# Kernel tuning notes

Measured on AMD Instinct MI355X. Metric: run time of the kernel, lower is better.

Reference implementation:

```python
import jax, jax.numpy as jnp
import numpy as np

SIZE = 1024      # codebook size
DIM = 64         # latent_dim
TOPK = 3
BETA_C = 0.25
LEGACY = False

def setup_inputs() -> dict:
    key = jax.random.key(0)
    kz, ke = jax.random.split(key)
    z = jax.random.normal(kz, (16, 64, 64, DIM), dtype=jnp.float32)
    # nn.Embedding init: uniform(-1/size, 1/size)
    emb = jax.random.uniform(ke, (SIZE, DIM), minval=-1.0 / SIZE, maxval=1.0 / SIZE, dtype=jnp.float32)
    return {"z": z, "emb": emb}

def reference(z, emb):
    zf = z.reshape(-1, DIM)                                  # [N, D]
    # squared euclidean distances via matmul expansion: [N, SIZE]
    d = (jnp.sum(zf ** 2, axis=1, keepdims=True)
         + jnp.sum(emb ** 2, axis=1)
         - 2.0 * (zf @ emb.T))
    neg_d, topk_idx = jax.lax.top_k(-d, TOPK)                # smallest distances -> [N, K]
    # direct gather instead of one-hot matmul (same math)
    z_q = jnp.mean(emb[topk_idx], axis=1).reshape(z.shape)   # [N,K,D] -> [N,D] -> z.shape
    if LEGACY:
        loss = (jnp.mean((jax.lax.stop_gradient(z_q) - z) ** 2)
                + BETA_C * jnp.mean((z_q - jax.lax.stop_gradient(z)) ** 2))
    else:
        loss = (BETA_C * jnp.mean((jax.lax.stop_gradient(z_q) - z) ** 2)
                + jnp.mean((z_q - jax.lax.stop_gradient(z)) ** 2))
    # one-hot encodings are part of the module's return signature
    topk_encodings = jax.nn.one_hot(topk_idx, SIZE, dtype=z.dtype)   # [N, K, SIZE]
    e_mean = jnp.mean(topk_encodings, axis=(0, 1))                   # [SIZE]
    perplexity = jnp.exp(-jnp.sum(e_mean * jnp.log(e_mean + 1e-10)))
    z_q_st = z + jax.lax.stop_gradient(z_q - z)              # straight-through estimator
    return (z_q_st, loss, perplexity, topk_encodings, topk_idx)
```

## Files before the change

### kernel.cpp

```cpp
#include <hip/hip_runtime.h>
#include <math.h>

#define N_ROWS 65536
#define CB 1024
#define SPLITS 4
#define JS (CB / SPLITS)

typedef float v4f __attribute__((ext_vector_type(4)));

__device__ __forceinline__ float tree_sum64_sq(const float* x) {
#pragma clang fp contract(off)
    float sq[64];
#pragma unroll
    for (int i = 0; i < 64; ++i) sq[i] = x[i] * x[i];
    float s[16];
#pragma unroll
    for (int l = 0; l < 16; ++l) s[l] = (sq[l] + sq[l + 16]) + (sq[l + 32] + sq[l + 48]);
    float t[8];
#pragma unroll
    for (int l = 0; l < 8; ++l) t[l] = s[l] + s[l + 8];
    float u[4];
#pragma unroll
    for (int l = 0; l < 4; ++l) u[l] = t[l] + t[l + 4];
    float v0 = u[0] + u[2];
    float v1 = u[1] + u[3];
    return v0 + v1;
}

__device__ __forceinline__ void top3_insert(float d, int j,
                                            float& v0, float& v1, float& v2,
                                            int& i0, int& i1, int& i2) {
    bool b0 = d < v0, b1 = d < v1, b2 = d < v2;
    v2 = b1 ? v1 : (b2 ? d : v2);
    i2 = b1 ? i1 : (b2 ? j : i2);
    v1 = b0 ? v0 : (b1 ? d : v1);
    i1 = b0 ? i0 : (b1 ? j : i1);
    v0 = b0 ? d : v0;
    i0 = b0 ? j : i0;
}

__global__ __launch_bounds__(256) void prep_kernel(const float* __restrict__ emb,
                                                   float* __restrict__ B,
                                                   int* __restrict__ hist,
                                                   float* __restrict__ lossAcc) {
    int j = blockIdx.x * 256 + threadIdx.x;
    if (j >= CB) return;
    float e[64];
    const float4* e4 = (const float4*)(emb + (size_t)j * 64);
#pragma unroll
    for (int k = 0; k < 16; ++k) {
        float4 v = e4[k];
        e[4 * k] = v.x; e[4 * k + 1] = v.y; e[4 * k + 2] = v.z; e[4 * k + 3] = v.w;
    }
    B[j] = tree_sum64_sq(e);
    hist[j] = 0;
    if (j == 0) *lossAcc = 0.0f;
}

__global__ __launch_bounds__(256) void score_kernel(const float* __restrict__ z,
                                                    const float* __restrict__ emb,
                                                    const float* __restrict__ B,
                                                    float* __restrict__ out0,
                                                    float* __restrict__ out3f,
                                                    float* __restrict__ out4,
                                                    int* __restrict__ hist,
                                                    float* __restrict__ lossAcc) {
    __shared__ float sD[SPLITS][64][3];
    __shared__ int   sI[SPLITS][64][3];

    int t = threadIdx.x;
    int r = t & 63;
    int split = __builtin_amdgcn_readfirstlane(t >> 6);
    int row = blockIdx.x * 64 + r;

    float zr[64];
    const float4* z4 = (const float4*)(z + (size_t)row * 64);
#pragma unroll
    for (int k = 0; k < 16; ++k) {
        float4 v = z4[k];
        zr[4 * k] = v.x; zr[4 * k + 1] = v.y; zr[4 * k + 2] = v.z; zr[4 * k + 3] = v.w;
    }
    float A = tree_sum64_sq(zr);

    float v0 = 3.402823466e38f, v1 = 3.402823466e38f, v2 = 3.402823466e38f;
    int i0 = 0, i1 = 0, i2 = 0;
    int jbase = split * JS;

#pragma unroll 2
    for (int jj = 0; jj < JS; ++jj) {
        int j = jbase + jj;
        const float4* e4 = (const float4*)(emb + (size_t)j * 64);
        float Bj = B[j];
        float acc = 0.0f;
#pragma unroll
        for (int k = 0; k < 16; ++k) {
            float4 e = e4[k];
            acc = fmaf(zr[4 * k],     e.x, acc);
            acc = fmaf(zr[4 * k + 1], e.y, acc);
            acc = fmaf(zr[4 * k + 2], e.z, acc);
            acc = fmaf(zr[4 * k + 3], e.w, acc);
        }
        float d = (A + Bj) - 2.0f * acc;
        top3_insert(d, j, v0, v1, v2, i0, i1, i2);
    }

    sD[split][r][0] = v0; sD[split][r][1] = v1; sD[split][r][2] = v2;
    sI[split][r][0] = i0; sI[split][r][1] = i1; sI[split][r][2] = i2;
    __syncthreads();

    if (t < 64) {
        float m0 = 3.402823466e38f, m1 = 3.402823466e38f, m2 = 3.402823466e38f;
        int j0 = 0, j1 = 0, j2 = 0;
#pragma unroll
        for (int s = 0; s < SPLITS; ++s) {
#pragma unroll
            for (int u = 0; u < 3; ++u)
                top3_insert(sD[s][r][u], sI[s][r][u], m0, m1, m2, j0, j1, j2);
        }

        size_t sb = (size_t)row * 3 * 1024;
        out3f[sb + j0]        = 1.0f;
        out3f[sb + 1024 + j1] = 1.0f;
        out3f[sb + 2048 + j2] = 1.0f;

        const float4* e0q = (const float4*)(emb + (size_t)j0 * 64);
        const float4* e1q = (const float4*)(emb + (size_t)j1 * 64);
        const float4* e2q = (const float4*)(emb + (size_t)j2 * 64);
        v4f* o4 = (v4f*)(out0 + (size_t)row * 64);

        float lsum = 0.0f;
#pragma unroll
        for (int k4 = 0; k4 < 16; ++k4) {
            float4 a = e0q[k4], b = e1q[k4], c = e2q[k4];
            float zx = zr[4 * k4], zy = zr[4 * k4 + 1];
            float zz = zr[4 * k4 + 2], zw = zr[4 * k4 + 3];
            v4f st;
            float zq, df;
            zq = ((a.x + b.x) + c.x) / 3.0f; df = zq - zx; st.x = zx + df; lsum = fmaf(df, df, lsum);
            zq = ((a.y + b.y) + c.y) / 3.0f; df = zq - zy; st.y = zy + df; lsum = fmaf(df, df, lsum);
            zq = ((a.z + b.z) + c.z) / 3.0f; df = zq - zz; st.z = zz + df; lsum = fmaf(df, df, lsum);
            zq = ((a.w + b.w) + c.w) / 3.0f; df = zq - zw; st.w = zw + df; lsum = fmaf(df, df, lsum);
            o4[k4] = st;
        }

        size_t ob = (size_t)row * 3;
        out4[ob]     = (float)j0;
        out4[ob + 1] = (float)j1;
        out4[ob + 2] = (float)j2;
        atomicAdd(&hist[j0], 1);
        atomicAdd(&hist[j1], 1);
        atomicAdd(&hist[j2], 1);

#pragma unroll
        for (int off = 32; off >= 1; off >>= 1) lsum += __shfl_down(lsum, off);
        if ((t & 63) == 0) atomicAdd(lossAcc, lsum);
    }
}

__global__ __launch_bounds__(256) void finalize_kernel(const int* __restrict__ hist,
                                                       const float* __restrict__ lossAcc,
                                                       float* __restrict__ out1,
                                                       float* __restrict__ out2) {
    __shared__ float red[256];
    int t = threadIdx.x;
    float local = 0.0f;
    for (int b = t; b < CB; b += 256) {
        float em = (float)hist[b] / 196608.0f;
        local += em * logf(em + 1e-10f);
    }
    red[t] = local;
    __syncthreads();
    for (int s = 128; s >= 1; s >>= 1) {
        if (t < s) red[t] += red[t + s];
        __syncthreads();
    }
    if (t == 0) {
        *out2 = expf(-red[0]);
        float m = *lossAcc / 4194304.0f;
        *out1 = 0.25f * m + m;
    }
}

extern "C" void kernel_launch(void* const* d_in, const int* in_sizes, int n_in,
                              void* d_out, int out_size, void* d_ws, size_t ws_size,
                              hipStream_t stream) {
    const float* z   = (const float*)d_in[0];
    const float* emb = (const float*)d_in[1];

    float* out  = (float*)d_out;
    float* out0 = out;
    float* out1 = out + 4194304;
    float* out2 = out + 4194305;
    float* out3 = out + 4194306;
    float* out4 = out + 4194306 + 201326592ll;

    int*   hist    = (int*)d_ws;
    float* lossAcc = (float*)((char*)d_ws + 4096);
    float* B       = (float*)((char*)d_ws + 8192);

    prep_kernel<<<4, 256, 0, stream>>>(emb, B, hist, lossAcc);
    hipMemsetAsync(out3, 0, (size_t)N_ROWS * 3 * CB * sizeof(float), stream);
    score_kernel<<<N_ROWS / 64, 256, 0, stream>>>(z, emb, B, out0, out3, out4,
                                                  hist, lossAcc);
    finalize_kernel<<<1, 256, 0, stream>>>(hist, lossAcc, out1, out2);
}
```

Before: 1.092 ms.

## Overlap one-hot zero-fill with scoring via filler blocks and per-slice flags

Drops the separate hipMemsetAsync of the large one-hot output and folds the zeroing into the main kernel. Extra filler blocks zero 4 row-group slices each, so the compute-bound scoring overlaps the bandwidth-bound fill. Per-slice flags and acquire/release atomics order the zeroing before the one-hot writes. If a filler has not claimed a slice in time, the scoring block takes it over and writes the full one-hot rows itself. This adds spin-wait synchronization, a launch_bounds occupancy hint, and the risk of stalls or deadlock if fillers are scheduled late.

New measurement: 1.201 ms. 1.1x slower.

```diff
diff --git a/kernel.cpp b/kernel.cpp
--- a/kernel.cpp
+++ b/kernel.cpp
@@ -5,6 +5,8 @@
 #define CB 1024
 #define SPLITS 4
 #define JS (CB / SPLITS)
+#define NFILLER 256
+#define SLICE_F 196608
 
 typedef float v4f __attribute__((ext_vector_type(4)));
 
@@ -42,7 +44,8 @@
 __global__ __launch_bounds__(256) void prep_kernel(const float* __restrict__ emb,
                                                    float* __restrict__ B,
                                                    int* __restrict__ hist,
-                                                   float* __restrict__ lossAcc) {
+                                                   float* __restrict__ lossAcc,
+                                                   int* __restrict__ flags) {
     int j = blockIdx.x * 256 + threadIdx.x;
     if (j >= CB) return;
     float e[64];
@@ -54,24 +57,60 @@
     }
     B[j] = tree_sum64_sq(e);
     hist[j] = 0;
+    flags[j] = 0;
     if (j == 0) *lossAcc = 0.0f;
 }
 
-__global__ __launch_bounds__(256) void score_kernel(const float* __restrict__ z,
-                                                    const float* __restrict__ emb,
-                                                    const float* __restrict__ B,
-                                                    float* __restrict__ out0,
-                                                    float* __restrict__ out3f,
-                                                    float* __restrict__ out4,
-                                                    int* __restrict__ hist,
-                                                    float* __restrict__ lossAcc) {
+__global__ __launch_bounds__(256, 5) void main_kernel(const float* __restrict__ z,
+                                                      const float* __restrict__ emb,
+                                                      const float* __restrict__ B,
+                                                      float* __restrict__ out0,
+                                                      float* __restrict__ out3f,
+                                                      float* __restrict__ out4,
+                                                      int* __restrict__ hist,
+                                                      float* __restrict__ lossAcc,
+                                                      int* __restrict__ flags) {
+    int bid = blockIdx.x;
+    int t = threadIdx.x;
+
+    if (bid < NFILLER) {
+        __shared__ int fown[4];
+        if (t == 0) {
+#pragma unroll
+            for (int q = 0; q < 4; ++q)
+                fown[q] = (atomicCAS(&flags[bid * 4 + q], 0, 3) == 0) ? 1 : 0;
+        }
+        __syncthreads();
+        v4f zz = {0.0f, 0.0f, 0.0f, 0.0f};
+        for (int q = 0; q < 4; ++q) {
+            if (!fown[q]) continue;
+            float* Sb = out3f + (size_t)(bid * 4 + q) * SLICE_F;
+            v4f* S4 = (v4f*)(Sb + 2);
+            for (int m = t; m < 49151; m += 256) S4[m] = zz;
+            if (t == 0) {
+                Sb[0] = 0.0f; Sb[1] = 0.0f;
+                Sb[SLICE_F - 2] = 0.0f; Sb[SLICE_F - 1] = 0.0f;
+            }
+        }
+        __syncthreads();
+        if (t == 0) {
+            __threadfence();
+#pragma unroll
+            for (int q = 0; q < 4; ++q)
+                if (fown[q])
+                    __hip_atomic_store(&flags[bid * 4 + q], 1,
+                                       __ATOMIC_RELEASE, __HIP_MEMORY_SCOPE_AGENT);
+        }
+        return;
+    }
+
     __shared__ float sD[SPLITS][64][3];
     __shared__ int   sI[SPLITS][64][3];
 
-    int t = threadIdx.x;
+    int g = bid - NFILLER;
     int r = t & 63;
     int split = __builtin_amdgcn_readfirstlane(t >> 6);
-    int row = blockIdx.x * 64 + r;
+    int row = g * 64 + r;
 
     float zr[64];
     const float4* z4 = (const float4*)(z + (size_t)row * 64);
@@ -118,11 +157,6 @@
                 top3_insert(sD[s][r][u], sI[s][r][u], m0, m1, m2, j0, j1, j2);
         }
 
-        size_t sb = (size_t)row * 3 * 1024;
-        out3f[sb + j0]        = 1.0f;
-        out3f[sb + 1024 + j1] = 1.0f;
-        out3f[sb + 2048 + j2] = 1.0f;
-
         const float4* e0q = (const float4*)(emb + (size_t)j0 * 64);
         const float4* e1q = (const float4*)(emb + (size_t)j1 * 64);
         const float4* e2q = (const float4*)(emb + (size_t)j2 * 64);
@@ -133,13 +167,13 @@
         for (int k4 = 0; k4 < 16; ++k4) {
             float4 a = e0q[k4], b = e1q[k4], c = e2q[k4];
             float zx = zr[4 * k4], zy = zr[4 * k4 + 1];
-            float zz = zr[4 * k4 + 2], zw = zr[4 * k4 + 3];
+            float zz2 = zr[4 * k4 + 2], zw = zr[4 * k4 + 3];
             v4f st;
             float zq, df;
-            zq = ((a.x + b.x) + c.x) / 3.0f; df = zq - zx; st.x = zx + df; lsum = fmaf(df, df, lsum);
-            zq = ((a.y + b.y) + c.y) / 3.0f; df = zq - zy; st.y = zy + df; lsum = fmaf(df, df, lsum);
-            zq = ((a.z + b.z) + c.z) / 3.0f; df = zq - zz; st.z = zz + df; lsum = fmaf(df, df, lsum);
-            zq = ((a.w + b.w) + c.w) / 3.0f; df = zq - zw; st.w = zw + df; lsum = fmaf(df, df, lsum);
+            zq = ((a.x + b.x) + c.x) / 3.0f; df = zq - zx;  st.x = zx  + df; lsum = fmaf(df, df, lsum);
+            zq = ((a.y + b.y) + c.y) / 3.0f; df = zq - zy;  st.y = zy  + df; lsum = fmaf(df, df, lsum);
+            zq = ((a.z + b.z) + c.z) / 3.0f; df = zq - zz2; st.z = zz2 + df; lsum = fmaf(df, df, lsum);
+            zq = ((a.w + b.w) + c.w) / 3.0f; df = zq - zw;  st.w = zw  + df; lsum = fmaf(df, df, lsum);
             o4[k4] = st;
         }
 
@@ -153,7 +187,50 @@
 
 #pragma unroll
         for (int off = 32; off >= 1; off >>= 1) lsum += __shfl_down(lsum, off);
-        if ((t & 63) == 0) atomicAdd(lossAcc, lsum);
+        if (r == 0) atomicAdd(lossAcc, lsum);
+
+        int selfown = 0;
+        if (r == 0) {
+            int it = 0;
+            while (1) {
+                int v = __hip_atomic_load(&flags[g], __ATOMIC_ACQUIRE,
+                                          __HIP_MEMORY_SCOPE_AGENT);
+                if (v == 1) break;
+                if (v == 0 && ++it > 1500) {
+                    int old = atomicCAS(&flags[g], 0, 2);
+                    if (old == 0) { selfown = 1; break; }
+                    if (old == 1) break;
+                    it = 0;
+                }
+                __builtin_amdgcn_s_sleep(10);
+            }
+        }
+        selfown = __shfl(selfown, 0);
+        __threadfence();
+
+        if (selfown) {
+            float* P = out3f + (size_t)g * SLICE_F + (size_t)r * 3072;
+            int o0 = j0, o1 = 1024 + j1, o2 = 2048 + j2;
+            P[0] = (o0 == 0) ? 1.0f : 0.0f;
+            P[1] = (o0 == 1) ? 1.0f : 0.0f;
+            v4f* P4 = (v4f*)(P + 2);
+            for (int m = 0; m < 767; ++m) {
+                int e = 2 + 4 * m;
+                v4f w;
+                w.x = (e     == o0 || e     == o1 || e     == o2) ? 1.0f : 0.0f;
+                w.y = (e + 1 == o0 || e + 1 == o1 || e + 1 == o2) ? 1.0f : 0.0f;
+                w.z = (e + 2 == o0 || e + 2 == o1 || e + 2 == o2) ? 1.0f : 0.0f;
+                w.w = (e + 3 == o0 || e + 3 == o1 || e + 3 == o2) ? 1.0f : 0.0f;
+                P4[m] = w;
+            }
+            P[3070] = (3070 == o2) ? 1.0f : 0.0f;
+            P[3071] = (3071 == o2) ? 1.0f : 0.0f;
+        } else {
+            size_t sb = (size_t)row * 3072;
+            out3f[sb + j0]        = 1.0f;
+            out3f[sb + 1024 + j1] = 1.0f;
+            out3f[sb + 2048 + j2] = 1.0f;
+        }
     }
 }
 
@@ -197,10 +274,10 @@
     int*   hist    = (int*)d_ws;
     float* lossAcc = (float*)((char*)d_ws + 4096);
     float* B       = (float*)((char*)d_ws + 8192);
-
-    prep_kernel<<<4, 256, 0, stream>>>(emb, B, hist, lossAcc);
-    hipMemsetAsync(out3, 0, (size_t)N_ROWS * 3 * CB * sizeof(float), stream);
-    score_kernel<<<N_ROWS / 64, 256, 0, stream>>>(z, emb, B, out0, out3, out4,
-                                                  hist, lossAcc);
+    int*   flags   = (int*)((char*)d_ws + 12288);
+
+    prep_kernel<<<4, 256, 0, stream>>>(emb, B, hist, lossAcc, flags);
+    main_kernel<<<NFILLER + N_ROWS / 64, 256, 0, stream>>>(z, emb, B, out0, out3,
+                                                           out4, hist, lossAcc, flags);
     finalize_kernel<<<1, 256, 0, stream>>>(hist, lossAcc, out1, out2);
 }
```

## Stage codebook chunks in LDS with prefetch, one row per thread

Applied to the files above, without the earlier changes.

Each thread now scans the full codebook for its own row instead of splitting the codebook across four thread groups and merging partial top-3 lists in shared memory. Codebook rows are staged in 64-entry chunks into LDS, with the next chunk prefetched into registers while the current one is scored. This replaces per-thread global/cache reads of the embeddings with broadcast LDS reads and removes the split merge. The cost is fewer blocks (256 rows per block, so 256 blocks in total), which may reduce occupancy and latency hiding, plus two barriers per chunk. It also adds a second accumulator chain per pair of codes.

Result: slower. 1.196 ms (+9.5%).

```diff
diff --git a/kernel.cpp b/kernel.cpp
--- a/kernel.cpp
+++ b/kernel.cpp
@@ -3,8 +3,6 @@
 
 #define N_ROWS 65536
 #define CB 1024
-#define SPLITS 4
-#define JS (CB / SPLITS)
 
 typedef float v4f __attribute__((ext_vector_type(4)));
 
@@ -65,13 +63,11 @@
                                                     float* __restrict__ out4,
                                                     int* __restrict__ hist,
                                                     float* __restrict__ lossAcc) {
-    __shared__ float sD[SPLITS][64][3];
-    __shared__ int   sI[SPLITS][64][3];
+    __shared__ float eL[4096];
+    __shared__ float eB[64];
 
     int t = threadIdx.x;
-    int r = t & 63;
-    int split = __builtin_amdgcn_readfirstlane(t >> 6);
-    int row = blockIdx.x * 64 + r;
+    int row = blockIdx.x * 256 + t;
 
     float zr[64];
     const float4* z4 = (const float4*)(z + (size_t)row * 64);
@@ -84,77 +80,93 @@
 
     float v0 = 3.402823466e38f, v1 = 3.402823466e38f, v2 = 3.402823466e38f;
     int i0 = 0, i1 = 0, i2 = 0;
-    int jbase = split * JS;
-
-#pragma unroll 2
-    for (int jj = 0; jj < JS; ++jj) {
-        int j = jbase + jj;
-        const float4* e4 = (const float4*)(emb + (size_t)j * 64);
-        float Bj = B[j];
-        float acc = 0.0f;
-#pragma unroll
-        for (int k = 0; k < 16; ++k) {
-            float4 e = e4[k];
-            acc = fmaf(zr[4 * k],     e.x, acc);
-            acc = fmaf(zr[4 * k + 1], e.y, acc);
-            acc = fmaf(zr[4 * k + 2], e.z, acc);
-            acc = fmaf(zr[4 * k + 3], e.w, acc);
+
+    const v4f* emb4 = (const v4f*)emb;
+    v4f pre[4];
+#pragma unroll
+    for (int q = 0; q < 4; ++q)
+        pre[q] = emb4[q * 256 + t];
+    float preB = (t < 64) ? B[t] : 0.0f;
+
+    for (int c = 0; c < 16; ++c) {
+        __syncthreads();
+#pragma unroll
+        for (int q = 0; q < 4; ++q)
+            ((v4f*)eL)[q * 256 + t] = pre[q];
+        if (t < 64) eB[t] = preB;
+        __syncthreads();
+        if (c < 15) {
+#pragma unroll
+            for (int q = 0; q < 4; ++q)
+                pre[q] = emb4[(c + 1) * 1024 + q * 256 + t];
+            if (t < 64) preB = B[(c + 1) * 64 + t];
         }
-        float d = (A + Bj) - 2.0f * acc;
-        top3_insert(d, j, v0, v1, v2, i0, i1, i2);
-    }
-
-    sD[split][r][0] = v0; sD[split][r][1] = v1; sD[split][r][2] = v2;
-    sI[split][r][0] = i0; sI[split][r][1] = i1; sI[split][r][2] = i2;
-    __syncthreads();
-
-    if (t < 64) {
-        float m0 = 3.402823466e38f, m1 = 3.402823466e38f, m2 = 3.402823466e38f;
-        int j0 = 0, j1 = 0, j2 = 0;
-#pragma unroll
-        for (int s = 0; s < SPLITS; ++s) {
-#pragma unroll
-            for (int u = 0; u < 3; ++u)
-                top3_insert(sD[s][r][u], sI[s][r][u], m0, m1, m2, j0, j1, j2);
+
+        for (int jj = 0; jj < 64; jj += 2) {
+            const float* e0 = eL + jj * 64;
+            const float* e1 = e0 + 64;
+            float Bj0 = eB[jj];
+            float Bj1 = eB[jj + 1];
+            float acc0 = 0.0f, acc1 = 0.0f;
+#pragma unroll
+            for (int k4 = 0; k4 < 16; ++k4) {
+                v4f a = *(const v4f*)(e0 + 4 * k4);
+                v4f b = *(const v4f*)(e1 + 4 * k4);
+                acc0 = fmaf(zr[4 * k4],     a.x, acc0);
+                acc1 = fmaf(zr[4 * k4],     b.x, acc1);
+                acc0 = fmaf(zr[4 * k4 + 1], a.y, acc0);
+                acc1 = fmaf(zr[4 * k4 + 1], b.y, acc1);
+                acc0 = fmaf(zr[4 * k4 + 2], a.z, acc0);
+                acc1 = fmaf(zr[4 * k4 + 2], b.z, acc1);
+                acc0 = fmaf(zr[4 * k4 + 3], a.w, acc0);
+                acc1 = fmaf(zr[4 * k4 + 3], b.w, acc1);
+            }
+            int j = c * 64 + jj;
+            float d0 = (A + Bj0) - 2.0f * acc0;
+            float d1 = (A + Bj1) - 2.0f * acc1;
+            top3_insert(d0, j,     v0, v1, v2, i0, i1, i2);
+            top3_insert(d1, j + 1, v0, v1, v2, i0, i1, i2);
         }
-
-        size_t sb = (size_t)row * 3 * 1024;
-        out3f[sb + j0]        = 1.0f;
-        out3f[sb + 1024 + j1] = 1.0f;
-        out3f[sb + 2048 + j2] = 1.0f;
-
-        const float4* e0q = (const float4*)(emb + (size_t)j0 * 64);
-        const float4* e1q = (const float4*)(emb + (size_t)j1 * 64);
-        const float4* e2q = (const float4*)(emb + (size_t)j2 * 64);
-        v4f* o4 = (v4f*)(out0 + (size_t)row * 64);
-
-        float lsum = 0.0f;
-#pragma unroll
-        for (int k4 = 0; k4 < 16; ++k4) {
-            float4 a = e0q[k4], b = e1q[k4], c = e2q[k4];
-            float zx = zr[4 * k4], zy = zr[4 * k4 + 1];
-            float zz = zr[4 * k4 + 2], zw = zr[4 * k4 + 3];
-            v4f st;
-            float zq, df;
-            zq = ((a.x + b.x) + c.x) / 3.0f; df = zq - zx; st.x = zx + df; lsum = fmaf(df, df, lsum);
-            zq = ((a.y + b.y) + c.y) / 3.0f; df = zq - zy; st.y = zy + df; lsum = fmaf(df, df, lsum);
-            zq = ((a.z + b.z) + c.z) / 3.0f; df = zq - zz; st.z = zz + df; lsum = fmaf(df, df, lsum);
-            zq = ((a.w + b.w) + c.w) / 3.0f; df = zq - zw; st.w = zw + df; lsum = fmaf(df, df, lsum);
-            o4[k4] = st;
-        }
-
-        size_t ob = (size_t)row * 3;
-        out4[ob]     = (float)j0;
-        out4[ob + 1] = (float)j1;
-        out4[ob + 2] = (float)j2;
-        atomicAdd(&hist[j0], 1);
-        atomicAdd(&hist[j1], 1);
-        atomicAdd(&hist[j2], 1);
-
-#pragma unroll
-        for (int off = 32; off >= 1; off >>= 1) lsum += __shfl_down(lsum, off);
-        if ((t & 63) == 0) atomicAdd(lossAcc, lsum);
-    }
+    }
+
+    int j0 = i0, j1 = i1, j2 = i2;
+
+    size_t sb = (size_t)row * 3072;
+    out3f[sb + j0]        = 1.0f;
+    out3f[sb + 1024 + j1] = 1.0f;
+    out3f[sb + 2048 + j2] = 1.0f;
+
+    const float4* e0q = (const float4*)(emb + (size_t)j0 * 64);
+    const float4* e1q = (const float4*)(emb + (size_t)j1 * 64);
+    const float4* e2q = (const float4*)(emb + (size_t)j2 * 64);
+    v4f* o4 = (v4f*)(out0 + (size_t)row * 64);
+
+    float lsum = 0.0f;
+#pragma unroll
+    for (int k4 = 0; k4 < 16; ++k4) {
+        float4 a = e0q[k4], b = e1q[k4], cc = e2q[k4];
+        float zx = zr[4 * k4], zy = zr[4 * k4 + 1];
+        float zz = zr[4 * k4 + 2], zw = zr[4 * k4 + 3];
+        v4f st;
+        float zq, df;
+        zq = ((a.x + b.x) + cc.x) / 3.0f; df = zq - zx; st.x = zx + df; lsum = fmaf(df, df, lsum);
+        zq = ((a.y + b.y) + cc.y) / 3.0f; df = zq - zy; st.y = zy + df; lsum = fmaf(df, df, lsum);
+        zq = ((a.z + b.z) + cc.z) / 3.0f; df = zq - zz; st.z = zz + df; lsum = fmaf(df, df, lsum);
+        zq = ((a.w + b.w) + cc.w) / 3.0f; df = zq - zw; st.w = zw + df; lsum = fmaf(df, df, lsum);
+        o4[k4] = st;
+    }
+
+    size_t ob = (size_t)row * 3;
+    out4[ob]     = (float)j0;
+    out4[ob + 1] = (float)j1;
+    out4[ob + 2] = (float)j2;
+    atomicAdd(&hist[j0], 1);
+    atomicAdd(&hist[j1], 1);
+    atomicAdd(&hist[j2], 1);
+
+#pragma unroll
+    for (int off = 32; off >= 1; off >>= 1) lsum += __shfl_down(lsum, off);
+    if ((t & 63) == 0) atomicAdd(lossAcc, lsum);
 }
 
 __global__ __launch_bounds__(256) void finalize_kernel(const int* __restrict__ hist,
@@ -200,7 +212,7 @@
 
     prep_kernel<<<4, 256, 0, stream>>>(emb, B, hist, lossAcc);
     hipMemsetAsync(out3, 0, (size_t)N_ROWS * 3 * CB * sizeof(float), stream);
-    score_kernel<<<N_ROWS / 64, 256, 0, stream>>>(z, emb, B, out0, out3, out4,
-                                                  hist, lossAcc);
+    score_kernel<<<N_ROWS / 256, 256, 0, stream>>>(z, emb, B, out0, out3, out4,
+                                                   hist, lossAcc);
     finalize_kernel<<<1, 256, 0, stream>>>(hist, lossAcc, out1, out2);
 }
```

## Register-block four rows per thread in score kernel to reuse codebook loads

Applied to the files above, without the earlier changes.

Each thread now computes distances for four z rows against its codebook slice, so each loaded embedding vector feeds four FMA chains. The grid is cut to 256-row blocks, and all four waves take part in the merge and epilogue instead of only the first. This trades heavy register use and low occupancy (launch bounds of 256 threads, one block) for fewer loads per FMA and more instruction-level parallelism.

Result: slower. 1.334 ms (+22.1%).

```diff
diff --git a/kernel.cpp b/kernel.cpp
--- a/kernel.cpp
+++ b/kernel.cpp
@@ -39,6 +39,16 @@
     i0 = b0 ? j : i0;
 }
 
+__device__ __forceinline__ void load_row(const float* __restrict__ z, int row,
+                                         float* zr) {
+    const float4* z4 = (const float4*)(z + (size_t)row * 64);
+#pragma unroll
+    for (int k = 0; k < 16; ++k) {
+        float4 v = z4[k];
+        zr[4 * k] = v.x; zr[4 * k + 1] = v.y; zr[4 * k + 2] = v.z; zr[4 * k + 3] = v.w;
+    }
+}
+
 __global__ __launch_bounds__(256) void prep_kernel(const float* __restrict__ emb,
                                                    float* __restrict__ B,
                                                    int* __restrict__ hist,
@@ -46,115 +56,147 @@
     int j = blockIdx.x * 256 + threadIdx.x;
     if (j >= CB) return;
     float e[64];
-    const float4* e4 = (const float4*)(emb + (size_t)j * 64);
-#pragma unroll
-    for (int k = 0; k < 16; ++k) {
-        float4 v = e4[k];
-        e[4 * k] = v.x; e[4 * k + 1] = v.y; e[4 * k + 2] = v.z; e[4 * k + 3] = v.w;
-    }
+    load_row(emb, j, e);
     B[j] = tree_sum64_sq(e);
     hist[j] = 0;
     if (j == 0) *lossAcc = 0.0f;
 }
 
-__global__ __launch_bounds__(256) void score_kernel(const float* __restrict__ z,
-                                                    const float* __restrict__ emb,
-                                                    const float* __restrict__ B,
-                                                    float* __restrict__ out0,
-                                                    float* __restrict__ out3f,
-                                                    float* __restrict__ out4,
-                                                    int* __restrict__ hist,
-                                                    float* __restrict__ lossAcc) {
-    __shared__ float sD[SPLITS][64][3];
-    __shared__ int   sI[SPLITS][64][3];
+__device__ __forceinline__ float epilogue_row(const float* zr, int row,
+                                              int j0, int j1, int j2,
+                                              const float* __restrict__ emb,
+                                              float* __restrict__ out0,
+                                              float* __restrict__ out3f,
+                                              float* __restrict__ out4,
+                                              int* __restrict__ hist) {
+    size_t sb = (size_t)row * 3072;
+    out3f[sb + j0]        = 1.0f;
+    out3f[sb + 1024 + j1] = 1.0f;
+    out3f[sb + 2048 + j2] = 1.0f;
+
+    const float4* e0q = (const float4*)(emb + (size_t)j0 * 64);
+    const float4* e1q = (const float4*)(emb + (size_t)j1 * 64);
+    const float4* e2q = (const float4*)(emb + (size_t)j2 * 64);
+    v4f* o4 = (v4f*)(out0 + (size_t)row * 64);
+
+    float lsum = 0.0f;
+#pragma unroll
+    for (int k4 = 0; k4 < 16; ++k4) {
+        float4 a = e0q[k4], b = e1q[k4], cc = e2q[k4];
+        float zx = zr[4 * k4], zy = zr[4 * k4 + 1];
+        float zz = zr[4 * k4 + 2], zw = zr[4 * k4 + 3];
+        v4f st;
+        float zq, df;
+        zq = ((a.x + b.x) + cc.x) / 3.0f; df = zq - zx; st.x = zx + df; lsum = fmaf(df, df, lsum);
+        zq = ((a.y + b.y) + cc.y) / 3.0f; df = zq - zy; st.y = zy + df; lsum = fmaf(df, df, lsum);
+        zq = ((a.z + b.z) + cc.z) / 3.0f; df = zq - zz; st.z = zz + df; lsum = fmaf(df, df, lsum);
+        zq = ((a.w + b.w) + cc.w) / 3.0f; df = zq - zw; st.w = zw + df; lsum = fmaf(df, df, lsum);
+        o4[k4] = st;
+    }
+
+    size_t ob = (size_t)row * 3;
+    out4[ob]     = (float)j0;
+    out4[ob + 1] = (float)j1;
+    out4[ob + 2] = (float)j2;
+    atomicAdd(&hist[j0], 1);
+    atomicAdd(&hist[j1], 1);
+    atomicAdd(&hist[j2], 1);
+    return lsum;
+}
+
+__global__ __launch_bounds__(256, 1) void score_kernel(const float* __restrict__ z,
+                                                       const float* __restrict__ emb,
+                                                       const float* __restrict__ B,
+                                                       float* __restrict__ out0,
+                                                       float* __restrict__ out3f,
+                                                       float* __restrict__ out4,
+                                                       int* __restrict__ hist,
+                                                       float* __restrict__ lossAcc) {
+    __shared__ float sD[SPLITS][4][64][3];
+    __shared__ int   sI[SPLITS][4][64][3];
 
     int t = threadIdx.x;
-    int r = t & 63;
-    int split = __builtin_amdgcn_readfirstlane(t >> 6);
-    int row = blockIdx.x * 64 + r;
-
-    float zr[64];
-    const float4* z4 = (const float4*)(z + (size_t)row * 64);
-#pragma unroll
-    for (int k = 0; k < 16; ++k) {
-        float4 v = z4[k];
-        zr[4 * k] = v.x; zr[4 * k + 1] = v.y; zr[4 * k + 2] = v.z; zr[4 * k + 3] = v.w;
-    }
-    float A = tree_sum64_sq(zr);
-
-    float v0 = 3.402823466e38f, v1 = 3.402823466e38f, v2 = 3.402823466e38f;
-    int i0 = 0, i1 = 0, i2 = 0;
-    int jbase = split * JS;
-
-#pragma unroll 2
+    int l = t & 63;
+    int w = __builtin_amdgcn_readfirstlane(t >> 6);
+    int rbase = blockIdx.x * 256;
+
+    float zr0[64], zr1[64], zr2[64], zr3[64];
+    load_row(z, rbase + l,       zr0);  float A0 = tree_sum64_sq(zr0);
+    load_row(z, rbase + l + 64,  zr1);  float A1 = tree_sum64_sq(zr1);
+    load_row(z, rbase + l + 128, zr2);  float A2 = tree_sum64_sq(zr2);
+    load_row(z, rbase + l + 192, zr3);  float A3 = tree_sum64_sq(zr3);
+
+    float tv[4][3];
+    int   ti[4][3];
+#pragma unroll
+    for (int q = 0; q < 4; ++q) {
+        tv[q][0] = tv[q][1] = tv[q][2] = 3.402823466e38f;
+        ti[q][0] = ti[q][1] = ti[q][2] = 0;
+    }
+
+    int jbase = w * JS;
     for (int jj = 0; jj < JS; ++jj) {
         int j = jbase + jj;
         const float4* e4 = (const float4*)(emb + (size_t)j * 64);
         float Bj = B[j];
-        float acc = 0.0f;
-#pragma unroll
-        for (int k = 0; k < 16; ++k) {
-            float4 e = e4[k];
-            acc = fmaf(zr[4 * k],     e.x, acc);
-            acc = fmaf(zr[4 * k + 1], e.y, acc);
-            acc = fmaf(zr[4 * k + 2], e.z, acc);
-            acc = fmaf(zr[4 * k + 3], e.w, acc);
+        float acc0 = 0.0f, acc1 = 0.0f, acc2 = 0.0f, acc3 = 0.0f;
+#pragma unroll
+        for (int k4 = 0; k4 < 16; ++k4) {
+            float4 e = e4[k4];
+            acc0 = fmaf(zr0[4 * k4],     e.x, acc0);
+            acc1 = fmaf(zr1[4 * k4],     e.x, acc1);
+            acc2 = fmaf(zr2[4 * k4],     e.x, acc2);
+            acc3 = fmaf(zr3[4 * k4],     e.x, acc3);
+            acc0 = fmaf(zr0[4 * k4 + 1], e.y, acc0);
+            acc1 = fmaf(zr1[4 * k4 + 1], e.y, acc1);
+            acc2 = fmaf(zr2[4 * k4 + 1], e.y, acc2);
+            acc3 = fmaf(zr3[4 * k4 + 1], e.y, acc3);
+            acc0 = fmaf(zr0[4 * k4 + 2], e.z, acc0);
+            acc1 = fmaf(zr1[4 * k4 + 2], e.z, acc1);
+            acc2 = fmaf(zr2[4 * k4 + 2], e.z, acc2);
+            acc3 = fmaf(zr3[4 * k4 + 2], e.z, acc3);
+            acc0 = fmaf(zr0[4 * k4 + 3], e.w, acc0);
+            acc1 = fmaf(zr1[4 * k4 + 3], e.w, acc1);
+            acc2 = fmaf(zr2[4 * k4 + 3], e.w, acc2);
+            acc3 = fmaf(zr3[4 * k4 + 3], e.w, acc3);
         }
-        float d = (A + Bj) - 2.0f * acc;
-        top3_insert(d, j, v0, v1, v2, i0, i1, i2);
-    }
-
-    sD[split][r][0] = v0; sD[split][r][1] = v1; sD[split][r][2] = v2;
-    sI[split][r][0] = i0; sI[split][r][1] = i1; sI[split][r][2] = i2;
+        float d0 = (A0 + Bj) - 2.0f * acc0;
+        float d1 = (A1 + Bj) - 2.0f * acc1;
+        float d2 = (A2 + Bj) - 2.0f * acc2;
+        float d3 = (A3 + Bj) - 2.0f * acc3;
+        top3_insert(d0, j, tv[0][0], tv[0][1], tv[0][2], ti[0][0], ti[0][1], ti[0][2]);
+        top3_insert(d1, j, tv[1][0], tv[1][1], tv[1][2], ti[1][0], ti[1][1], ti[1][2]);
+        top3_insert(d2, j, tv[2][0], tv[2][1], tv[2][2], ti[2][0], ti[2][1], ti[2][2]);
+        top3_insert(d3, j, tv[3][0], tv[3][1], tv[3][2], ti[3][0], ti[3][1], ti[3][2]);
+    }
+
+#pragma unroll
+    for (int q = 0; q < 4; ++q)
+#pragma unroll
+        for (int u = 0; u < 3; ++u) {
+            sD[w][q][l][u] = tv[q][u];
+            sI[w][q][l][u] = ti[q][u];
+        }
     __syncthreads();
 
-    if (t < 64) {
-        float m0 = 3.402823466e38f, m1 = 3.402823466e38f, m2 = 3.402823466e38f;
-        int j0 = 0, j1 = 0, j2 = 0;
-#pragma unroll
-        for (int s = 0; s < SPLITS; ++s) {
-#pragma unroll
-            for (int u = 0; u < 3; ++u)
-                top3_insert(sD[s][r][u], sI[s][r][u], m0, m1, m2, j0, j1, j2);
-        }
-
-        size_t sb = (size_t)row * 3 * 1024;
-        out3f[sb + j0]        = 1.0f;
-        out3f[sb + 1024 + j1] = 1.0f;
-        out3f[sb + 2048 + j2] = 1.0f;
-
-        const float4* e0q = (const float4*)(emb + (size_t)j0 * 64);
-        const float4* e1q = (const float4*)(emb + (size_t)j1 * 64);
-        const float4* e2q = (const float4*)(emb + (size_t)j2 * 64);
-        v4f* o4 = (v4f*)(out0 + (size_t)row * 64);
-
-        float lsum = 0.0f;
-#pragma unroll
-        for (int k4 = 0; k4 < 16; ++k4) {
-            float4 a = e0q[k4], b = e1q[k4], c = e2q[k4];
-            float zx = zr[4 * k4], zy = zr[4 * k4 + 1];
-            float zz = zr[4 * k4 + 2], zw = zr[4 * k4 + 3];
-            v4f st;
-            float zq, df;
-            zq = ((a.x + b.x) + c.x) / 3.0f; df = zq - zx; st.x = zx + df; lsum = fmaf(df, df, lsum);
-            zq = ((a.y + b.y) + c.y) / 3.0f; df = zq - zy; st.y = zy + df; lsum = fmaf(df, df, lsum);
-            zq = ((a.z + b.z) + c.z) / 3.0f; df = zq - zz; st.z = zz + df; lsum = fmaf(df, df, lsum);
-            zq = ((a.w + b.w) + c.w) / 3.0f; df = zq - zw; st.w = zw + df; lsum = fmaf(df, df, lsum);
-            o4[k4] = st;
-        }
-
-        size_t ob = (size_t)row * 3;
-        out4[ob]     = (float)j0;
-        out4[ob + 1] = (float)j1;
-        out4[ob + 2] = (float)j2;
-        atomicAdd(&hist[j0], 1);
-        atomicAdd(&hist[j1], 1);
-        atomicAdd(&hist[j2], 1);
-
-#pragma unroll
-        for (int off = 32; off >= 1; off >>= 1) lsum += __shfl_down(lsum, off);
-        if ((t & 63) == 0) atomicAdd(lossAcc, lsum);
-    }
+    float m0 = 3.402823466e38f, m1 = 3.402823466e38f, m2 = 3.402823466e38f;
+    int j0 = 0, j1 = 0, j2 = 0;
+#pragma unroll
+    for (int s = 0; s < SPLITS; ++s)
+#pragma unroll
+        for (int u = 0; u < 3; ++u)
+            top3_insert(sD[s][w][l][u], sI[s][w][l][u], m0, m1, m2, j0, j1, j2);
+
+    int row = rbase + w * 64 + l;
+    float lsum;
+    if      (w == 0) lsum = epilogue_row(zr0, row, j0, j1, j2, emb, out0, out3f, out4, hist);
+    else if (w == 1) lsum = epilogue_row(zr1, row, j0, j1, j2, emb, out0, out3f, out4, hist);
+    else if (w == 2) lsum = epilogue_row(zr2, row, j0, j1, j2, emb, out0, out3f, out4, hist);
+    else             lsum = epilogue_row(zr3, row, j0, j1, j2, emb, out0, out3f, out4, hist);
+
+#pragma unroll
+    for (int off = 32; off >= 1; off >>= 1) lsum += __shfl_down(lsum, off);
+    if (l == 0) atomicAdd(lossAcc, lsum);
 }
 
 __global__ __launch_bounds__(256) void finalize_kernel(const int* __restrict__ hist,
@@ -200,7 +242,7 @@
 
     prep_kernel<<<4, 256, 0, stream>>>(emb, B, hist, lossAcc);
     hipMemsetAsync(out3, 0, (size_t)N_ROWS * 3 * CB * sizeof(float), stream);
-    score_kernel<<<N_ROWS / 64, 256, 0, stream>>>(z, emb, B, out0, out3, out4,
-                                                  hist, lossAcc);
+    score_kernel<<<N_ROWS / 256, 256, 0, stream>>>(z, emb, B, out0, out3, out4,
+                                                   hist, lossAcc);
     finalize_kernel<<<1, 256, 0, stream>>>(hist, lossAcc, out1, out2);
 }
```
